# Performance work log

Measured on AMD Instinct MI355X. Metric: run time of the kernel, lower is better.

## Reference

```python
import jax, jax.numpy as jnp
import numpy as np

B, P, M, C = 8, 131072, 16, 2
THRESHOLD = 0.5
GAMMA = 2.0
ALPHA_W = 0.25  # focal 'weight' for the foreground class


def _cxcycz_to_xyz(b):
    return jnp.concatenate([b[..., :3] - b[..., 3:] / 2, b[..., :3] + b[..., 3:] / 2], -1)


def _xyz_to_cxcycz(b):
    return jnp.concatenate([(b[..., :3] + b[..., 3:]) / 2, b[..., 3:] - b[..., :3]], -1)


def _encode(cxcycz, priors_cxcycz):
    # standard SSD encoding with variances (10, 5), extended to 3D
    return jnp.concatenate([
        (cxcycz[..., :3] - priors_cxcycz[..., :3]) / (priors_cxcycz[..., 3:] / 10.0),
        jnp.log(cxcycz[..., 3:] / priors_cxcycz[..., 3:]) * 5.0], -1)


def _jaccard3d(a, b):
    # a: [M,6] xyz boxes, b: [P,6] xyz boxes -> [M,P] IoU
    lo = jnp.maximum(a[:, None, :3], b[None, :, :3])
    hi = jnp.minimum(a[:, None, 3:], b[None, :, 3:])
    inter = jnp.prod(jnp.clip(hi - lo, 0.0, None), -1)
    va = jnp.prod(a[:, 3:] - a[:, :3], -1)
    vb = jnp.prod(b[:, 3:] - b[:, :3], -1)
    return inter / (va[:, None] + vb[None, :] - inter)


def setup_inputs():
    key = jax.random.key(0)
    k1, k2, k3, k4, k5, k6 = jax.random.split(key, 6)
    predicted_locs = jax.random.normal(k1, (B, P, 6), jnp.float32)
    predicted_scores = jax.random.normal(k2, (B, P, C), jnp.float32)
    # valid ground-truth boxes in boundary (xyz) coords inside unit cube
    ctr = jax.random.uniform(k3, (B, M, 3)) * 0.8 + 0.1
    sz = jax.random.uniform(k4, (B, M, 3)) * 0.15 + 0.05
    boxes = jnp.concatenate([ctr - sz / 2, ctr + sz / 2], -1)
    # priors in center-size (cxcycz) coords
    pctr = jax.random.uniform(k5, (P, 3)) * 0.9 + 0.05
    psz = jax.random.uniform(k6, (P, 3)) * 0.2 + 0.03
    priors_cxcycz = jnp.concatenate([pctr, psz], -1)
    labels = jnp.ones((B, M), jnp.int32)  # single foreground class
    return dict(predicted_locs=predicted_locs, predicted_scores=predicted_scores,
                boxes=boxes, labels=labels, priors_cxcycz=priors_cxcycz)


def _forward(predicted_locs, predicted_scores, boxes, priors_cxcycz, labels):
    priors_xyz = _cxcycz_to_xyz(priors_cxcycz)

    def match(boxes_i, labels_i):
        ov = _jaccard3d(boxes_i, priors_xyz)           # [M, P]
        overlap_fep = ov.max(0)                        # [P] best IoU per prior
        object_fep = ov.argmax(0)                      # [P] best object per prior
        prior_feo = ov.argmax(1)                       # [M] best prior per object
        # force each object to own its best prior
        object_fep = object_fep.at[prior_feo].set(jnp.arange(M))
        overlap_fep = overlap_fep.at[prior_feo].set(1.0)
        lab = labels_i[object_fep]
        lab = jnp.where(overlap_fep < THRESHOLD, 0, lab)  # hard thresholding
        tl = _encode(_xyz_to_cxcycz(boxes_i[object_fep]), priors_cxcycz)
        return lab, tl

    true_classes, true_locs = jax.vmap(match)(boxes, labels)  # [B,P], [B,P,6]

    pos = true_classes > 0
    n_pos = pos.sum()
    # nn.L1Loss() = mean over all selected elements (n_pos priors x 6 coords)
    diff = jnp.abs(predicted_locs - true_locs) * pos[..., None].astype(predicted_locs.dtype)
    loc_loss = jnp.where(n_pos > 0,
                         diff.sum() / jnp.maximum(n_pos.astype(jnp.float32) * 6.0, 1.0),
                         jnp.float32(0.0))

    # sigmoid focal loss on foreground channel (include_background=False, C==2)
    x = predicted_scores[..., 1]                       # [B,P] fg logit
    t = pos.astype(x.dtype)
    ce = -(t * jax.nn.log_sigmoid(x) + (1.0 - t) * jax.nn.log_sigmoid(-x))
    p = jax.nn.sigmoid(x)
    pt = jnp.where(pos, p, 1.0 - p)
    focal = (ALPHA_W * t + (1.0 - ALPHA_W) * (1.0 - t)) * (1.0 - pt) ** GAMMA * ce
    conf_loss = focal.mean()
    return conf_loss, loc_loss


def reference(predicted_locs, predicted_scores, boxes, labels, priors_cxcycz):
    return _forward(predicted_locs, predicted_scores, boxes, priors_cxcycz, labels)
```

## Files before the change

### kernel.cpp

```cpp
#include <hip/hip_runtime.h>

#define NB 8
#define NP 131072
#define NM 16
#define THRESH 0.5f
#define BLK 256
#define PPT 2
#define PPB (BLK * PPT)
#define BPB (NP / PPB)
#define NPAIR (NB * NM)
#define NBLOCKS (NB * BPB)

typedef unsigned long long u64;
typedef unsigned int u32;


template <int CTRL>
__device__ __forceinline__ float dppmv(float x) {
    return __int_as_float(__builtin_amdgcn_update_dpp(
        0, __float_as_int(x), CTRL, 0xf, 0xf, false));
}

__device__ __forceinline__ float wave_max63(float x) {
    x = fmaxf(x, dppmv<0x111>(x));
    x = fmaxf(x, dppmv<0x112>(x));
    x = fmaxf(x, dppmv<0x114>(x));
    x = fmaxf(x, dppmv<0x118>(x));
    x = fmaxf(x, dppmv<0x142>(x));
    x = fmaxf(x, dppmv<0x143>(x));
    return x;
}

__device__ __forceinline__ float wave_sum63(float x) {
    x += dppmv<0x111>(x);
    x += dppmv<0x112>(x);
    x += dppmv<0x114>(x);
    x += dppmv<0x118>(x);
    x += dppmv<0x142>(x);
    x += dppmv<0x143>(x);
    return x;
}

__device__ __forceinline__ float bcast63(float x) {
    return __int_as_float(__builtin_amdgcn_readlane(__float_as_int(x), 63));
}


__device__ __forceinline__ float iou_term(float inter, float va, float vb) {
    return (inter > 0.0f) ? inter * __builtin_amdgcn_rcpf(va + vb - inter) : 0.0f;
}

__device__ __forceinline__ float iou_box(const float4 A, const float4 B4,
                                         const float pl[3], const float ph[3],
                                         float vb) {
    float d0 = fminf(A.w,  ph[0]) - fmaxf(A.x, pl[0]);
    float d1 = fminf(B4.x, ph[1]) - fmaxf(A.y, pl[1]);
    float d2 = fminf(B4.y, ph[2]) - fmaxf(A.z, pl[2]);
    float inter = fmaxf(d0, 0.0f) * fmaxf(d1, 0.0f) * fmaxf(d2, 0.0f);
    return iou_term(inter, B4.z, vb);
}

__device__ __forceinline__ float focal_term(float x, bool pos) {
    float t = __expf(-fabsf(x));
    float r = __builtin_amdgcn_rcpf(1.0f + t);
    float L = __logf(1.0f + t);
    float ce = (pos ? fmaxf(-x, 0.0f) : fmaxf(x, 0.0f)) + L;
    float omp = (pos == (x >= 0.0f)) ? t * r : r;
    float w = pos ? 0.25f : 0.75f;
    return w * omp * omp * ce;
}

__device__ __forceinline__ float l1_enc(const float* lp,
                                        const float blo[3], const float bhi[3],
                                        const float pc[3], const float ps[3]) {
    float s = 0.0f;
#pragma unroll
    for (int k = 0; k < 3; ++k) {
        float gc = (blo[k] + bhi[k]) / 2.0f;
        float gs = bhi[k] - blo[k];
        float e  = (gc - pc[k]) / (ps[k] / 10.0f);
        float e2 = __logf(gs / ps[k]) * 5.0f;
        s += fabsf(lp[k]     - e);
        s += fabsf(lp[3 + k] - e2);
    }
    return s;
}

__device__ __forceinline__ u32 decode_p(u64 k) { return ~(u32)(k & 0xFFFFFFFFull); }


__global__ __launch_bounds__(BLK) void match_loss_kernel(
        const float* __restrict__ locs, const float* __restrict__ scores,
        const float* __restrict__ boxes, const int* __restrict__ labels,
        const float* __restrict__ priors,
        u64* __restrict__ keys_out,
        float4* __restrict__ part) {
    __shared__ float4 s_box[NM][2];
    __shared__ u64    s_wkey[4][NM];
    __shared__ float  s_wred[4][3];

    const int tid  = threadIdx.x;
    const int b    = blockIdx.y;
    const int lane = tid & 63, wave = tid >> 6;
    const int p0   = blockIdx.x * PPB + 2 * tid;
    const int p1   = p0 + 1;

    if (tid < NM) {
        const float* bx = &boxes[(b * NM + tid) * 6];
        float l0 = bx[0], l1 = bx[1], l2 = bx[2];
        float h0 = bx[3], h1 = bx[4], h2 = bx[5];
        s_box[tid][0] = make_float4(l0, l1, l2, h0);
        float va = (h0 - l0) * (h1 - l1) * (h2 - l2);
        s_box[tid][1] = make_float4(h1, h2, va, __int_as_float(labels[b * NM + tid]));
    }
    __syncthreads();

    const float4* pr4 = reinterpret_cast<const float4*>(priors);
    const size_t f4b = (size_t)(p0 / 2) * 3;
    float4 q0 = pr4[f4b + 0], q1 = pr4[f4b + 1], q2 = pr4[f4b + 2];
    const float pc0[3] = {q0.x, q0.y, q0.z}, ps0[3] = {q0.w, q1.x, q1.y};
    const float pc1[3] = {q1.z, q1.w, q2.x}, ps1[3] = {q2.y, q2.z, q2.w};
    float pl0[3], ph0[3], pl1[3], ph1[3];
#pragma unroll
    for (int k = 0; k < 3; ++k) {
        pl0[k] = pc0[k] - ps0[k] / 2.0f; ph0[k] = pc0[k] + ps0[k] / 2.0f;
        pl1[k] = pc1[k] - ps1[k] / 2.0f; ph1[k] = pc1[k] + ps1[k] / 2.0f;
    }
    const float vb0 = (ph0[0] - pl0[0]) * (ph0[1] - pl0[1]) * (ph0[2] - pl0[2]);
    const float vb1 = (ph1[0] - pl1[0]) * (ph1[1] - pl1[1]) * (ph1[2] - pl1[2]);

    float best0 = -1.0f, best1 = -1.0f; int bm0 = 0, bm1 = 0;
#pragma unroll
    for (int m = 0; m < NM; ++m) {
        float4 A = s_box[m][0], B4 = s_box[m][1];
        float i0 = iou_box(A, B4, pl0, ph0, vb0);
        float i1 = iou_box(A, B4, pl1, ph1, vb1);
        if (i0 > best0) { best0 = i0; bm0 = m; }
        if (i1 > best1) { best1 = i1; bm1 = m; }
        float ci = i0; u32 cp = (u32)p0;
        if (i1 > ci) { ci = i1; cp = (u32)p1; }
        float wm = bcast63(wave_max63(ci));
        u64 eq = __ballot(ci == wm);
        int ls = __ffsll(eq) - 1;
        u32 wp = (u32)__builtin_amdgcn_readlane((int)cp, ls);
        if (lane == 0)
            s_wkey[wave][m] = ((u64)__float_as_uint(wm) << 32) | (u32)~wp;
    }

    const float4 sc = reinterpret_cast<const float4*>(scores)[((size_t)b * NP + p0) >> 1];
    float4 A0 = s_box[bm0][0], B0 = s_box[bm0][1];
    float4 A1 = s_box[bm1][0], B1 = s_box[bm1][1];
    const bool pos0 = (best0 >= THRESH) && (__float_as_int(B0.w) > 0);
    const bool pos1 = (best1 >= THRESH) && (__float_as_int(B1.w) > 0);
    float f = focal_term(sc.y, pos0) + focal_term(sc.w, pos1);
    float l = 0.0f;
    if (pos0) {
        float blo[3] = {A0.x, A0.y, A0.z}, bhi[3] = {A0.w, B0.x, B0.y};
        l += l1_enc(&locs[((size_t)b * NP + p0) * 6], blo, bhi, pc0, ps0);
    }
    if (pos1) {
        float blo[3] = {A1.x, A1.y, A1.z}, bhi[3] = {A1.w, B1.x, B1.y};
        l += l1_enc(&locs[((size_t)b * NP + p1) * 6], blo, bhi, pc1, ps1);
    }
    float n = (pos0 ? 1.0f : 0.0f) + (pos1 ? 1.0f : 0.0f);

    f = wave_sum63(f); l = wave_sum63(l); n = wave_sum63(n);
    if (lane == 63) { s_wred[wave][0] = f; s_wred[wave][1] = l; s_wred[wave][2] = n; }
    __syncthreads();

    if (tid < NM) {
        u64 k = s_wkey[0][tid];
#pragma unroll
        for (int w = 1; w < 4; ++w) k = (s_wkey[w][tid] > k) ? s_wkey[w][tid] : k;
        keys_out[(size_t)(b * NM + tid) * BPB + blockIdx.x] = k;
    }
    if (tid == 0) {
        part[b * BPB + blockIdx.x] =
            make_float4(s_wred[0][0] + s_wred[1][0] + s_wred[2][0] + s_wred[3][0],
                        s_wred[0][1] + s_wred[1][1] + s_wred[2][1] + s_wred[3][1],
                        s_wred[0][2] + s_wred[1][2] + s_wred[2][2] + s_wred[3][2],
                        0.0f);
    }
}


__global__ __launch_bounds__(1024) void finalize_kernel(
        const float* __restrict__ locs, const float* __restrict__ scores,
        const float* __restrict__ boxes, const int* __restrict__ labels,
        const float* __restrict__ priors, const u64* __restrict__ keys_in,
        const float4* __restrict__ part, float* __restrict__ out) {
    __shared__ u64   s_key[NPAIR];
    __shared__ float s_red[16][3];
    __shared__ float s_fix[16][3];
    const int t = threadIdx.x, lane = t & 63, wave = t >> 6;

    float f = 0.0f, l = 0.0f, n = 0.0f;
    for (int i = t; i < NBLOCKS; i += 1024) {
        float4 v = part[i]; f += v.x; l += v.y; n += v.z;
    }
    f = wave_sum63(f); l = wave_sum63(l); n = wave_sum63(n);
    if (lane == 63) { s_red[wave][0] = f; s_red[wave][1] = l; s_red[wave][2] = n; }

#pragma unroll
    for (int i = 0; i < 8; ++i) {
        const int pair = wave * 8 + i;
        const u64* kp = keys_in + (size_t)pair * BPB;
        u64 k = 0;
#pragma unroll
        for (int j = 0; j < BPB / 64; ++j) {
            u64 v = kp[j * 64 + lane];
            k = (v > k) ? v : k;
        }
#pragma unroll
        for (int off = 32; off > 0; off >>= 1) {
            u64 o = __shfl_down(k, off);
            k = (o > k) ? o : k;
        }
        if (lane == 0) s_key[pair] = k;
    }
    __syncthreads();

    float df = 0.0f, dl = 0.0f, dn = 0.0f;
    if (t < NPAIR) {
        const int b = t / NM, m = t % NM;
        const u32 pstar = decode_p(s_key[t]);
        bool skip = false;
        for (int mm = m + 1; mm < NM; ++mm)
            skip |= (decode_p(s_key[b * NM + mm]) == pstar);
        if (!skip) {
            const int p = (int)pstar;
            float pc[3], ps[3], pl[3], ph[3];
#pragma unroll
            for (int k = 0; k < 3; ++k) { pc[k] = priors[p * 6 + k]; ps[k] = priors[p * 6 + 3 + k]; }
#pragma unroll
            for (int k = 0; k < 3; ++k) { pl[k] = pc[k] - ps[k] / 2.0f; ph[k] = pc[k] + ps[k] / 2.0f; }
            const float vb = (ph[0] - pl[0]) * (ph[1] - pl[1]) * (ph[2] - pl[2]);

            float best = -1.0f; int bestm = 0;
            for (int mm = 0; mm < NM; ++mm) {
                const float* bx = &boxes[(b * NM + mm) * 6];
                float d0 = fminf(bx[3], ph[0]) - fmaxf(bx[0], pl[0]);
                float d1 = fminf(bx[4], ph[1]) - fmaxf(bx[1], pl[1]);
                float d2 = fminf(bx[5], ph[2]) - fmaxf(bx[2], pl[2]);
                float inter = fmaxf(d0, 0.0f) * fmaxf(d1, 0.0f) * fmaxf(d2, 0.0f);
                float va = (bx[3] - bx[0]) * (bx[4] - bx[1]) * (bx[5] - bx[2]);
                float iou = iou_term(inter, va, vb);
                if (iou > best) { best = iou; bestm = mm; }
            }
            const bool old_pos = (best >= THRESH) && (labels[b * NM + bestm] > 0);
            const bool new_pos = (labels[b * NM + m] > 0);

            const float x = scores[((size_t)b * NP + p) * 2 + 1];
            df = focal_term(x, new_pos) - focal_term(x, old_pos);
            dn = (new_pos ? 1.0f : 0.0f) - (old_pos ? 1.0f : 0.0f);

            const float* lp = &locs[((size_t)b * NP + p) * 6];
            if (new_pos) {
                const float* bx = &boxes[(b * NM + m) * 6];
                float blo[3] = {bx[0], bx[1], bx[2]}, bhi[3] = {bx[3], bx[4], bx[5]};
                dl += l1_enc(lp, blo, bhi, pc, ps);
            }
            if (old_pos) {
                const float* bx = &boxes[(b * NM + bestm) * 6];
                float blo[3] = {bx[0], bx[1], bx[2]}, bhi[3] = {bx[3], bx[4], bx[5]};
                dl -= l1_enc(lp, blo, bhi, pc, ps);
            }
        }
    }
    df = wave_sum63(df); dl = wave_sum63(dl); dn = wave_sum63(dn);
    if (lane == 63) { s_fix[wave][0] = df; s_fix[wave][1] = dl; s_fix[wave][2] = dn; }
    __syncthreads();

    if (t == 0) {
        float tf = 0.0f, tl = 0.0f, tn = 0.0f;
        for (int w = 0; w < 16; ++w) {
            tf += s_red[w][0] + s_fix[w][0];
            tl += s_red[w][1] + s_fix[w][1];
            tn += s_red[w][2] + s_fix[w][2];
        }
        out[0] = tf / (float)(NB * NP);
        out[1] = (tn > 0.5f) ? tl / fmaxf(tn * 6.0f, 1.0f) : 0.0f;
    }
}


extern "C" void kernel_launch(void* const* d_in, const int* in_sizes, int n_in,
                              void* d_out, int out_size, void* d_ws, size_t ws_size,
                              hipStream_t stream) {
    const float* locs   = (const float*)d_in[0];
    const float* scores = (const float*)d_in[1];
    const float* boxes  = (const float*)d_in[2];
    const int*   labels = (const int*)d_in[3];
    const float* priors = (const float*)d_in[4];
    float* out = (float*)d_out;

    u64*    keys = (u64*)d_ws;
    float4* part = (float4*)((char*)d_ws + (size_t)NPAIR * BPB * 8);

    dim3 grid(BPB, NB);
    match_loss_kernel<<<grid, BLK, 0, stream>>>(locs, scores, boxes, labels, priors,
                                                keys, part);
    finalize_kernel<<<1, 1024, 0, stream>>>(locs, scores, boxes, labels, priors, keys,
                                            part, out);
}
```

Measured before the change: 36.73 us.

## Process four priors per thread and batch wave reductions after IoU loop

Each thread now handles four priors instead of two, which halves the block count and amortizes the per-gt-box wave max/ballot/readlane reduction over more priors. The IoU loop first stores per-box candidates in register arrays, then runs all sixteen wave reductions in a separate loop so that independent IoU math is not serialized behind the cross-lane ops. The trade-off is higher register pressure, fewer waves in flight, and a reload of prior centers from global memory for positive priors.

```diff
diff --git a/kernel.cpp b/kernel.cpp
--- a/kernel.cpp
+++ b/kernel.cpp
@@ -5,7 +5,7 @@
 #define NM 16
 #define THRESH 0.5f
 #define BLK 256
-#define PPT 2
+#define PPT 4
 #define PPB (BLK * PPT)
 #define BPB (NP / PPB)
 #define NPAIR (NB * NM)
@@ -102,8 +102,7 @@
     const int tid  = threadIdx.x;
     const int b    = blockIdx.y;
     const int lane = tid & 63, wave = tid >> 6;
-    const int p0   = blockIdx.x * PPB + 2 * tid;
-    const int p1   = p0 + 1;
+    const int p0   = blockIdx.x * PPB + PPT * tid;
 
     if (tid < NM) {
         const float* bx = &boxes[(b * NM + tid) * 6];
@@ -118,51 +117,78 @@
     const float4* pr4 = reinterpret_cast<const float4*>(priors);
     const size_t f4b = (size_t)(p0 / 2) * 3;
     float4 q0 = pr4[f4b + 0], q1 = pr4[f4b + 1], q2 = pr4[f4b + 2];
-    const float pc0[3] = {q0.x, q0.y, q0.z}, ps0[3] = {q0.w, q1.x, q1.y};
-    const float pc1[3] = {q1.z, q1.w, q2.x}, ps1[3] = {q2.y, q2.z, q2.w};
-    float pl0[3], ph0[3], pl1[3], ph1[3];
-#pragma unroll
-    for (int k = 0; k < 3; ++k) {
-        pl0[k] = pc0[k] - ps0[k] / 2.0f; ph0[k] = pc0[k] + ps0[k] / 2.0f;
-        pl1[k] = pc1[k] - ps1[k] / 2.0f; ph1[k] = pc1[k] + ps1[k] / 2.0f;
-    }
-    const float vb0 = (ph0[0] - pl0[0]) * (ph0[1] - pl0[1]) * (ph0[2] - pl0[2]);
-    const float vb1 = (ph1[0] - pl1[0]) * (ph1[1] - pl1[1]) * (ph1[2] - pl1[2]);
-
-    float best0 = -1.0f, best1 = -1.0f; int bm0 = 0, bm1 = 0;
+    float4 q3 = pr4[f4b + 3], q4 = pr4[f4b + 4], q5 = pr4[f4b + 5];
+    float pl[PPT][3], ph[PPT][3], vb[PPT];
+    {
+        const float qf[24] = {q0.x,q0.y,q0.z,q0.w, q1.x,q1.y,q1.z,q1.w,
+                              q2.x,q2.y,q2.z,q2.w, q3.x,q3.y,q3.z,q3.w,
+                              q4.x,q4.y,q4.z,q4.w, q5.x,q5.y,q5.z,q5.w};
+#pragma unroll
+        for (int j = 0; j < PPT; ++j) {
+#pragma unroll
+            for (int k = 0; k < 3; ++k) {
+                float c = qf[6 * j + k], s = qf[6 * j + 3 + k];
+                pl[j][k] = c - s / 2.0f;
+                ph[j][k] = c + s / 2.0f;
+            }
+            vb[j] = (ph[j][0] - pl[j][0]) * (ph[j][1] - pl[j][1]) * (ph[j][2] - pl[j][2]);
+        }
+    }
+
+    float ci[NM]; u32 cp[NM];
+    float best[PPT]; int bm[PPT];
+#pragma unroll
+    for (int j = 0; j < PPT; ++j) { best[j] = -1.0f; bm[j] = 0; }
 #pragma unroll
     for (int m = 0; m < NM; ++m) {
         float4 A = s_box[m][0], B4 = s_box[m][1];
-        float i0 = iou_box(A, B4, pl0, ph0, vb0);
-        float i1 = iou_box(A, B4, pl1, ph1, vb1);
-        if (i0 > best0) { best0 = i0; bm0 = m; }
-        if (i1 > best1) { best1 = i1; bm1 = m; }
-        float ci = i0; u32 cp = (u32)p0;
-        if (i1 > ci) { ci = i1; cp = (u32)p1; }
-        float wm = bcast63(wave_max63(ci));
-        u64 eq = __ballot(ci == wm);
+        float i0 = iou_box(A, B4, pl[0], ph[0], vb[0]);
+        float i1 = iou_box(A, B4, pl[1], ph[1], vb[1]);
+        float i2 = iou_box(A, B4, pl[2], ph[2], vb[2]);
+        float i3 = iou_box(A, B4, pl[3], ph[3], vb[3]);
+        if (i0 > best[0]) { best[0] = i0; bm[0] = m; }
+        if (i1 > best[1]) { best[1] = i1; bm[1] = m; }
+        if (i2 > best[2]) { best[2] = i2; bm[2] = m; }
+        if (i3 > best[3]) { best[3] = i3; bm[3] = m; }
+        float v = i0; u32 w = (u32)p0;
+        if (i1 > v) { v = i1; w = (u32)(p0 + 1); }
+        if (i2 > v) { v = i2; w = (u32)(p0 + 2); }
+        if (i3 > v) { v = i3; w = (u32)(p0 + 3); }
+        ci[m] = v; cp[m] = w;
+    }
+
+#pragma unroll
+    for (int m = 0; m < NM; ++m) {
+        float wm = bcast63(wave_max63(ci[m]));
+        u64 eq = __ballot(ci[m] == wm);
         int ls = __ffsll(eq) - 1;
-        u32 wp = (u32)__builtin_amdgcn_readlane((int)cp, ls);
+        u32 wp = (u32)__builtin_amdgcn_readlane((int)cp[m], ls);
         if (lane == 0)
             s_wkey[wave][m] = ((u64)__float_as_uint(wm) << 32) | (u32)~wp;
     }
 
-    const float4 sc = reinterpret_cast<const float4*>(scores)[((size_t)b * NP + p0) >> 1];
-    float4 A0 = s_box[bm0][0], B0 = s_box[bm0][1];
-    float4 A1 = s_box[bm1][0], B1 = s_box[bm1][1];
-    const bool pos0 = (best0 >= THRESH) && (__float_as_int(B0.w) > 0);
-    const bool pos1 = (best1 >= THRESH) && (__float_as_int(B1.w) > 0);
-    float f = focal_term(sc.y, pos0) + focal_term(sc.w, pos1);
-    float l = 0.0f;
-    if (pos0) {
-        float blo[3] = {A0.x, A0.y, A0.z}, bhi[3] = {A0.w, B0.x, B0.y};
-        l += l1_enc(&locs[((size_t)b * NP + p0) * 6], blo, bhi, pc0, ps0);
-    }
-    if (pos1) {
-        float blo[3] = {A1.x, A1.y, A1.z}, bhi[3] = {A1.w, B1.x, B1.y};
-        l += l1_enc(&locs[((size_t)b * NP + p1) * 6], blo, bhi, pc1, ps1);
-    }
-    float n = (pos0 ? 1.0f : 0.0f) + (pos1 ? 1.0f : 0.0f);
+    const float4* sc4 = reinterpret_cast<const float4*>(scores);
+    const size_t scb = ((size_t)b * NP + p0) >> 1;
+    float4 sA = sc4[scb], sB = sc4[scb + 1];
+    const float xs[PPT] = {sA.y, sA.w, sB.y, sB.w};
+
+    float f = 0.0f, l = 0.0f, n = 0.0f;
+#pragma unroll
+    for (int j = 0; j < PPT; ++j) {
+        float4 Bb = s_box[bm[j]][1];
+        const bool pos = (best[j] >= THRESH) && (__float_as_int(Bb.w) > 0);
+        f += focal_term(xs[j], pos);
+        if (pos) {
+            const int p = p0 + j;
+            float pc[3], ps[3];
+#pragma unroll
+            for (int k = 0; k < 3; ++k) { pc[k] = priors[p * 6 + k]; ps[k] = priors[p * 6 + 3 + k]; }
+            float4 Ab = s_box[bm[j]][0];
+            float blo[3] = {Ab.x, Ab.y, Ab.z}, bhi[3] = {Ab.w, Bb.x, Bb.y};
+            l += l1_enc(&locs[((size_t)b * NP + p) * 6], blo, bhi, pc, ps);
+            n += 1.0f;
+        }
+    }
 
     f = wave_sum63(f); l = wave_sum63(l); n = wave_sum63(n);
     if (lane == 63) { s_wred[wave][0] = f; s_wred[wave][1] = l; s_wred[wave][2] = n; }
```

Measured after the change: 34.48 us. 6.1% less time.
